# Performance work log

Measured on AMD Instinct MI355X. Metric: run time of the kernel, lower is better.

The kernel has to match this reference:

```python
import jax, jax.numpy as jnp
import numpy as np

OUTLINER_RATIO = 0.01
SUB_OUTLINER_BIT = 8
NEG_INF = -1e9


def setup_inputs() -> dict:
    key = jax.random.key(0)
    T, H, D = 4096, 8, 64
    qkv = jax.random.normal(key, (T, 3, H, D), dtype=jnp.float32)
    cu_seqlens = jnp.array([0, 1024, 2048, 3072, 4096], dtype=jnp.int32)
    return {"qkv": qkv, "cu_seqlens": cu_seqlens, "max_seqlen": 1024}


def _varlen_attention(q, k, v, cu_seqlens, causal=False):
    # q,k,v: [T, H, D]; sequences delimited by cu_seqlens (attention never
    # crosses segment boundaries, matching flash_attn_varlen semantics).
    T, H, D = q.shape
    scale = D ** (-0.5)
    pos = jnp.arange(T)
    seg = jnp.searchsorted(cu_seqlens, pos, side="right") - 1  # [T] segment ids
    mask = seg[:, None] == seg[None, :]                          # [T, T]
    if causal:
        mask = mask & (pos[:, None] >= pos[None, :])
    scores = jnp.einsum("thd,shd->hts", q, k) * scale            # [H, T, T]
    scores = jnp.where(mask[None, :, :], scores, NEG_INF)
    probs = jax.nn.softmax(scores, axis=-1)
    out = jnp.einsum("hts,shd->thd", probs, v)                   # [T, H, D]
    return out


def _outlier_quant_compress(x, outliner_ratio=OUTLINER_RATIO, bit=SUB_OUTLINER_BIT):
    # Outlier detection: keep top-ratio |x| entries in full precision;
    # quantize the residual (sub-outliers) to `bit` bits per-tensor.
    a = jnp.abs(x)
    thr = jnp.quantile(a.reshape(-1), 1.0 - outliner_ratio)
    outliers = jnp.where(a > thr, x, 0.0)
    resid = x - outliers
    qmax = 2.0 ** (bit - 1) - 1.0
    scale = jnp.maximum(jnp.max(jnp.abs(resid)), 1e-8) / qmax
    q = jnp.clip(jnp.round(resid / scale), -qmax, qmax)
    x_hat = outliers + q * scale  # decompressed approximation
    return x_hat, thr, scale


def reference(qkv, cu_seqlens, max_seqlen):
    q, k, v = qkv[:, 0], qkv[:, 1], qkv[:, 2]
    out = _varlen_attention(q, k, v, cu_seqlens, causal=False)
    # Compression pipeline (stats + quantize) runs on Q,K,V,O in the original
    # forward; it does not alter the forward output.
    for t in (q, k, v, out):
        _outlier_quant_compress(t)
    return out
```

## Files before the change

kernel.cpp:

```cpp
#include <hip/hip_runtime.h>


#define HEADS 8
#define DH 64
#define TQ 64
#define TK 64
#define PSTR 72
#define NSPLIT 2
#define NEG_BIG -1e30f
#define L2E 1.44269504088896340736f

using f32x4 = __attribute__((ext_vector_type(4))) float;
using s16x8 = __attribute__((ext_vector_type(8))) short;

__device__ inline unsigned short bf16b(float x) {
    union { float f; unsigned u; } c; c.f = x;
    unsigned r = c.u + 0x7fffu + ((c.u >> 16) & 1u);
    return (unsigned short)(r >> 16);
}

#if __has_builtin(__builtin_amdgcn_cvt_pk_bf16_f32)
__device__ inline unsigned pk2(float a, float b) {
    auto v = __builtin_amdgcn_cvt_pk_bf16_f32(a, b);
    unsigned u; __builtin_memcpy(&u, &v, 4); return u;
}
#else
__device__ inline unsigned pk2(float a, float b) {
    return (unsigned)bf16b(a) | ((unsigned)bf16b(b) << 16);
}
#endif

__global__ __launch_bounds__(256)
void prep_kernel(const float* __restrict__ qkv, unsigned short* __restrict__ Kb,
                 unsigned short* __restrict__ Vtb, int T) {
    __shared__ unsigned short Lt[64][PSTR];
    const int m = blockIdx.z + 1;
    const int h = blockIdx.y, t0 = blockIdx.x * 64;
    const int tid = threadIdx.x, d8 = tid & 7, tr = tid >> 3;

    #pragma unroll
    for (int i = 0; i < 2; ++i) {
        int t = t0 + i * 32 + tr;
        int tc = t < T ? t : T - 1;
        const float* src = qkv + ((size_t)tc * 3 + m) * (HEADS * DH) + h * DH + d8 * 8;
        float4 a = *(const float4*)src;
        float4 b = *(const float4*)(src + 4);
        unsigned p0 = pk2(a.x, a.y), p1 = pk2(a.z, a.w);
        unsigned p2 = pk2(b.x, b.y), p3 = pk2(b.z, b.w);
        if (m == 2) {
            *(uint2*)&Lt[i * 32 + tr][d8 * 8]     = make_uint2(p0, p1);
            *(uint2*)&Lt[i * 32 + tr][d8 * 8 + 4] = make_uint2(p2, p3);
        } else if (t < T) {
            *(uint4*)(Kb + ((size_t)h * T + t) * DH + d8 * 8) = make_uint4(p0, p1, p2, p3);
        }
    }
    if (m == 2) {
        __syncthreads();
        const int d = tid >> 2, tg = tid & 3;
        #pragma unroll
        for (int p = 0; p < 2; ++p) {
            int G = tg + 4 * p;
            int td = t0 + G * 8;
            unsigned u[4];
            #pragma unroll
            for (int jj = 0; jj < 4; ++jj)
                u[jj] = (unsigned)Lt[G * 8 + 2 * jj][d] |
                        ((unsigned)Lt[G * 8 + 2 * jj + 1][d] << 16);
            if (td < T)
                *(uint4*)(Vtb + ((size_t)h * DH + d) * T + td) =
                    make_uint4(u[0], u[1], u[2], u[3]);
        }
    }
}

__global__ __launch_bounds__(256, 3)
void fa_main(const float* __restrict__ qkv, const unsigned short* __restrict__ Kb,
             const unsigned short* __restrict__ Vtb, const int* __restrict__ cu,
             int n_cu, int T, float* __restrict__ out,
             float* __restrict__ Opart, float* __restrict__ Mp, float* __restrict__ Lp) {
    __shared__ unsigned short Ksh[2][TK * DH];
    __shared__ unsigned short Vsh[2][TK * DH];
    __shared__ unsigned short Psh[TQ][PSTR];

    const int tid = threadIdx.x;
    const int h = blockIdx.y, t0 = blockIdx.x * TQ;
    const int split = blockIdx.z, nsplit = gridDim.z;
    const int w = tid >> 6, lane = tid & 63, n15 = lane & 15, quad = lane >> 4;

    int trow = t0 + w * 16 + n15; if (trow > T - 1) trow = T - 1;
    int lo, hi;
    { int s = 0; for (int j = 1; j < n_cu - 1; ++j) if (cu[j] <= trow) s = j;
      lo = cu[s]; hi = cu[s + 1]; }
    int kb_, ke;
    { int s = 0; for (int j = 1; j < n_cu - 1; ++j) if (cu[j] <= t0) s = j;
      kb_ = cu[s];
      int tl = t0 + TQ - 1; if (tl > T - 1) tl = T - 1;
      s = 0; for (int j = 1; j < n_cu - 1; ++j) if (cu[j] <= tl) s = j;
      ke = cu[s + 1]; }

    s16x8 qfrag[2];
    {
        int tc = t0 + w * 16 + n15; if (tc > T - 1) tc = T - 1;
        const float* qp = qkv + (size_t)tc * 3 * (HEADS * DH) + h * DH + quad * 8;
        #pragma unroll
        for (int kh = 0; kh < 2; ++kh) {
            float4 a = *(const float4*)(qp + kh * 32);
            float4 b = *(const float4*)(qp + kh * 32 + 4);
            unsigned u0 = pk2(a.x * 0.125f, a.y * 0.125f);
            unsigned u1 = pk2(a.z * 0.125f, a.w * 0.125f);
            unsigned u2 = pk2(b.x * 0.125f, b.y * 0.125f);
            unsigned u3 = pk2(b.z * 0.125f, b.w * 0.125f);
            uint4 uu = make_uint4(u0, u1, u2, u3);
            __builtin_memcpy(&qfrag[kh], &uu, 16);
        }
    }

    const unsigned short* kb_h = Kb + (size_t)h * T * DH;
    const unsigned short* vt_h = Vtb + (size_t)h * DH * T;
    int krow_rel[2], vkey_off[2], ldst[2];
    const unsigned short* kbase[2];
    const unsigned short* vbase[2];
    #pragma unroll
    for (int i = 0; i < 2; ++i) {
        int gg = i * 64 + lane;
        int rr = gg >> 3;
        int gc = gg & 7;
        int row = w * 16 + rr;
        int gcol = gc ^ (row & 7);
        krow_rel[i] = row;
        kbase[i] = kb_h + gcol * 8;
        vbase[i] = vt_h + (size_t)row * T;
        vkey_off[i] = gcol * 8;
        ldst[i] = (w * 128 + i * 64) * 8;
    }
    int off16[2];
    #pragma unroll
    for (int kh = 0; kh < 2; ++kh)
        off16[kh] = n15 * 128 + (((kh * 4 + quad) ^ (n15 & 7)) * 16);

    f32x4 oacc[4];
    #pragma unroll
    for (int i = 0; i < 4; ++i) oacc[i] = (f32x4){0.f, 0.f, 0.f, 0.f};
    float m_ = NEG_BIG, l_ = 0.f;

    const int step = nsplit * TK;
    const int c0_start = (kb_ / TK) * TK + split * TK;

    #pragma unroll
    for (int i = 0; i < 2; ++i) {
        int rk = c0_start + krow_rel[i]; if (rk > T - 1) rk = T - 1;
        __builtin_amdgcn_global_load_lds(
            (const __attribute__((address_space(1))) void*)(kbase[i] + ((size_t)rk << 6)),
            (__attribute__((address_space(3))) void*)&Ksh[0][ldst[i]], 16, 0, 0);
        int kv = c0_start + vkey_off[i]; if (kv > T - 8) kv = T - 8;
        __builtin_amdgcn_global_load_lds(
            (const __attribute__((address_space(1))) void*)(vbase[i] + kv),
            (__attribute__((address_space(3))) void*)&Vsh[0][ldst[i]], 16, 0, 0);
    }

    int ib = 0;
    for (int c0 = c0_start; c0 < ke; c0 += step, ib ^= 1) {
        __syncthreads();

        int cn = c0 + step;
        if (cn < ke) {
            #pragma unroll
            for (int i = 0; i < 2; ++i) {
                int rk = cn + krow_rel[i]; if (rk > T - 1) rk = T - 1;
                __builtin_amdgcn_global_load_lds(
                    (const __attribute__((address_space(1))) void*)(kbase[i] + ((size_t)rk << 6)),
                    (__attribute__((address_space(3))) void*)&Ksh[ib ^ 1][ldst[i]], 16, 0, 0);
                int kv = cn + vkey_off[i]; if (kv > T - 8) kv = T - 8;
                __builtin_amdgcn_global_load_lds(
                    (const __attribute__((address_space(1))) void*)(vbase[i] + kv),
                    (__attribute__((address_space(3))) void*)&Vsh[ib ^ 1][ldst[i]], 16, 0, 0);
            }
        }

        const char* Kc = (const char*)Ksh[ib];
        f32x4 sacc[4];
        #pragma unroll
        for (int nt = 0; nt < 4; ++nt) {
            s16x8 k0 = *(const s16x8*)(Kc + nt * 2048 + off16[0]);
            s16x8 k1 = *(const s16x8*)(Kc + nt * 2048 + off16[1]);
            f32x4 z = (f32x4){0.f, 0.f, 0.f, 0.f};
            z = __builtin_amdgcn_mfma_f32_16x16x32_bf16(k0, qfrag[0], z, 0, 0, 0);
            z = __builtin_amdgcn_mfma_f32_16x16x32_bf16(k1, qfrag[1], z, 0, 0, 0);
            sacc[nt] = z;
        }

        if (!(c0 >= lo && c0 + TK <= hi)) {
            #pragma unroll
            for (int nt = 0; nt < 4; ++nt)
                #pragma unroll
                for (int reg = 0; reg < 4; ++reg) {
                    int key = c0 + nt * 16 + quad * 4 + reg;
                    bool valid = (key >= lo) && (key < hi);
                    sacc[nt][reg] = valid ? sacc[nt][reg] : NEG_BIG;
                }
        }

        float rm = NEG_BIG;
        #pragma unroll
        for (int nt = 0; nt < 4; ++nt)
            #pragma unroll
            for (int reg = 0; reg < 4; ++reg) rm = fmaxf(rm, sacc[nt][reg]);
        rm = fmaxf(rm, __shfl_xor(rm, 16));
        rm = fmaxf(rm, __shfl_xor(rm, 32));
        float mn = fmaxf(m_, rm);
        float alpha = exp2f((m_ - mn) * L2E);
        float mnl = mn * L2E;
        float rs = 0.f;
        #pragma unroll
        for (int nt = 0; nt < 4; ++nt) {
            float p0 = exp2f(fmaf(sacc[nt][0], L2E, -mnl));
            float p1 = exp2f(fmaf(sacc[nt][1], L2E, -mnl));
            float p2 = exp2f(fmaf(sacc[nt][2], L2E, -mnl));
            float p3 = exp2f(fmaf(sacc[nt][3], L2E, -mnl));
            rs += (p0 + p1) + (p2 + p3);
            *(uint2*)&Psh[w * 16 + n15][nt * 16 + quad * 4] =
                make_uint2(pk2(p0, p1), pk2(p2, p3));
        }
        rs += __shfl_xor(rs, 16);
        rs += __shfl_xor(rs, 32);
        l_ = fmaf(l_, alpha, rs);
        m_ = mn;
        #pragma unroll
        for (int reg = 0; reg < 4; ++reg) {
            float ar = __shfl(alpha, quad * 4 + reg);
            oacc[0][reg] *= ar; oacc[1][reg] *= ar;
            oacc[2][reg] *= ar; oacc[3][reg] *= ar;
        }

        s16x8 afr[2];
        afr[0] = *(const s16x8*)&Psh[w * 16 + n15][quad * 8];
        afr[1] = *(const s16x8*)&Psh[w * 16 + n15][32 + quad * 8];
        const char* Vc = (const char*)Vsh[ib];
        #pragma unroll
        for (int nt = 0; nt < 4; ++nt) {
            s16x8 v0 = *(const s16x8*)(Vc + nt * 2048 + off16[0]);
            s16x8 v1 = *(const s16x8*)(Vc + nt * 2048 + off16[1]);
            oacc[nt] = __builtin_amdgcn_mfma_f32_16x16x32_bf16(afr[0], v0, oacc[nt], 0, 0, 0);
            oacc[nt] = __builtin_amdgcn_mfma_f32_16x16x32_bf16(afr[1], v1, oacc[nt], 0, 0, 0);
        }
    }

    if (nsplit == 1) {
        #pragma unroll
        for (int reg = 0; reg < 4; ++reg) {
            float lr = __shfl(l_, quad * 4 + reg);
            float inv = 1.f / fmaxf(lr, 1e-30f);
            int t = t0 + w * 16 + quad * 4 + reg;
            if (t < T) {
                #pragma unroll
                for (int nt = 0; nt < 4; ++nt)
                    out[((size_t)t * HEADS + h) * DH + nt * 16 + n15] = oacc[nt][reg] * inv;
            }
        }
    } else {
        #pragma unroll
        for (int reg = 0; reg < 4; ++reg) {
            int t = t0 + w * 16 + quad * 4 + reg;
            if (t < T) {
                size_t base = (((size_t)split * T + t) * HEADS + h) * DH;
                #pragma unroll
                for (int nt = 0; nt < 4; ++nt)
                    Opart[base + nt * 16 + n15] = oacc[nt][reg];
            }
        }
        int tq = t0 + w * 16 + n15;
        if (quad == 0 && tq < T) {
            size_t mi = ((size_t)split * T + tq) * HEADS + h;
            Mp[mi] = m_; Lp[mi] = l_;
        }
    }
}

__global__ __launch_bounds__(256)
void fa_combine_kernel(const float* __restrict__ Opart, const float* __restrict__ Mp,
                       const float* __restrict__ Lp, float* __restrict__ out, int T) {
    int i4 = blockIdx.x * blockDim.x + threadIdx.x;
    int total = T * HEADS * (DH / 4);
    if (i4 >= total) return;
    int th = i4 / (DH / 4);
    int d4 = i4 - th * (DH / 4);
    size_t stride = (size_t)T * HEADS * DH;
    int mlstride = T * HEADS;
    float m[NSPLIT], l[NSPLIT];
    float M = NEG_BIG;
    #pragma unroll
    for (int s = 0; s < NSPLIT; ++s) {
        m[s] = Mp[(size_t)s * mlstride + th];
        l[s] = Lp[(size_t)s * mlstride + th];
        M = fmaxf(M, m[s]);
    }
    float L = 0.f, wgt[NSPLIT];
    #pragma unroll
    for (int s = 0; s < NSPLIT; ++s) {
        wgt[s] = exp2f((m[s] - M) * L2E);
        L = fmaf(l[s], wgt[s], L);
    }
    float inv = 1.f / fmaxf(L, 1e-30f);
    size_t off = (size_t)th * DH + 4 * d4;
    float4 o = make_float4(0.f, 0.f, 0.f, 0.f);
    #pragma unroll
    for (int s = 0; s < NSPLIT; ++s) {
        float4 a = *(const float4*)&Opart[(size_t)s * stride + off];
        float ws = wgt[s];
        o.x = fmaf(a.x, ws, o.x); o.y = fmaf(a.y, ws, o.y);
        o.z = fmaf(a.z, ws, o.z); o.w = fmaf(a.w, ws, o.w);
    }
    o.x *= inv; o.y *= inv; o.z *= inv; o.w *= inv;
    *(float4*)&out[off] = o;
}

extern "C" void kernel_launch(void* const* d_in, const int* in_sizes, int n_in,
                              void* d_out, int out_size, void* d_ws, size_t ws_size,
                              hipStream_t stream) {
    const float* qkv = (const float*)d_in[0];
    const int* cu    = (const int*)d_in[1];
    const int n_cu   = in_sizes[1];
    const int T      = in_sizes[0] / (3 * HEADS * DH);
    float* out       = (float*)d_out;

    size_t elems = (size_t)T * HEADS * DH;

    float* Opart = (float*)d_ws;
    float* Mpp   = Opart + (size_t)NSPLIT * elems;
    float* Lpp   = Mpp + (size_t)NSPLIT * T * HEADS;
    unsigned short* Kb  = (unsigned short*)(Lpp + (size_t)NSPLIT * T * HEADS);
    unsigned short* Vtb = Kb + elems;

    int ptiles = (T + 63) / 64;
    dim3 pgrid(ptiles, HEADS, 2);
    prep_kernel<<<pgrid, 256, 0, stream>>>(qkv, Kb, Vtb, T);

    int tiles = (T + TQ - 1) / TQ;
    dim3 grid(tiles, HEADS, NSPLIT);
    fa_main<<<grid, 256, 0, stream>>>(qkv, Kb, Vtb, cu, n_cu, T, out, Opart, Mpp, Lpp);

    int total4 = T * HEADS * (DH / 4);
    fa_combine_kernel<<<(total4 + 255) / 256, 256, 0, stream>>>(Opart, Mpp, Lpp, out, T);
}
```

Before: 109.4 us.

## Load K/V fragments directly from global into registers, drop LDS staging

Removes the double-buffered shared-memory staging of K and V tiles (global_load_lds plus syncthreads) and has each wave load its MFMA operand fragments straight from global memory into registers. Occupancy hint is raised from 3 to 4 blocks per CU since LDS use drops. This removes barrier and LDS traffic, but each of the 4 waves now fetches the same K/V tile separately, leaning on the L1/L2 caches. Prefetch overlap is also lost because the loads are issued in the same iteration they are consumed.

```diff
diff --git a/kernel.cpp b/kernel.cpp
--- a/kernel.cpp
+++ b/kernel.cpp
@@ -73,13 +73,11 @@
     }
 }
 
-__global__ __launch_bounds__(256, 3)
+__global__ __launch_bounds__(256, 4)
 void fa_main(const float* __restrict__ qkv, const unsigned short* __restrict__ Kb,
              const unsigned short* __restrict__ Vtb, const int* __restrict__ cu,
              int n_cu, int T, float* __restrict__ out,
              float* __restrict__ Opart, float* __restrict__ Mp, float* __restrict__ Lp) {
-    __shared__ unsigned short Ksh[2][TK * DH];
-    __shared__ unsigned short Vsh[2][TK * DH];
     __shared__ unsigned short Psh[TQ][PSTR];
 
     const int tid = threadIdx.x;
@@ -115,28 +113,11 @@
         }
     }
 
-    const unsigned short* kb_h = Kb + (size_t)h * T * DH;
-    const unsigned short* vt_h = Vtb + (size_t)h * DH * T;
-    int krow_rel[2], vkey_off[2], ldst[2];
-    const unsigned short* kbase[2];
-    const unsigned short* vbase[2];
-    #pragma unroll
-    for (int i = 0; i < 2; ++i) {
-        int gg = i * 64 + lane;
-        int rr = gg >> 3;
-        int gc = gg & 7;
-        int row = w * 16 + rr;
-        int gcol = gc ^ (row & 7);
-        krow_rel[i] = row;
-        kbase[i] = kb_h + gcol * 8;
-        vbase[i] = vt_h + (size_t)row * T;
-        vkey_off[i] = gcol * 8;
-        ldst[i] = (w * 128 + i * 64) * 8;
-    }
-    int off16[2];
-    #pragma unroll
-    for (int kh = 0; kh < 2; ++kh)
-        off16[kh] = n15 * 128 + (((kh * 4 + quad) ^ (n15 & 7)) * 16);
+    const unsigned short* kp_base = Kb + ((size_t)h * T + n15) * DH + quad * 8;
+    const unsigned short* vrow[4];
+    #pragma unroll
+    for (int nt = 0; nt < 4; ++nt)
+        vrow[nt] = Vtb + ((size_t)h * DH + nt * 16 + n15) * T;
 
     f32x4 oacc[4];
     #pragma unroll
@@ -146,46 +127,30 @@
     const int step = nsplit * TK;
     const int c0_start = (kb_ / TK) * TK + split * TK;
 
-    #pragma unroll
-    for (int i = 0; i < 2; ++i) {
-        int rk = c0_start + krow_rel[i]; if (rk > T - 1) rk = T - 1;
-        __builtin_amdgcn_global_load_lds(
-            (const __attribute__((address_space(1))) void*)(kbase[i] + ((size_t)rk << 6)),
-            (__attribute__((address_space(3))) void*)&Ksh[0][ldst[i]], 16, 0, 0);
-        int kv = c0_start + vkey_off[i]; if (kv > T - 8) kv = T - 8;
-        __builtin_amdgcn_global_load_lds(
-            (const __attribute__((address_space(1))) void*)(vbase[i] + kv),
-            (__attribute__((address_space(3))) void*)&Vsh[0][ldst[i]], 16, 0, 0);
-    }
-
-    int ib = 0;
-    for (int c0 = c0_start; c0 < ke; c0 += step, ib ^= 1) {
-        __syncthreads();
-
-        int cn = c0 + step;
-        if (cn < ke) {
+    for (int c0 = c0_start; c0 < ke; c0 += step) {
+        s16x8 kf[4][2];
+        #pragma unroll
+        for (int nt = 0; nt < 4; ++nt) {
+            int kk = c0 + nt * 16; if (kk > T - 16) kk = T - 16;
+            const unsigned short* kp = kp_base + (size_t)kk * DH;
+            kf[nt][0] = *(const s16x8*)kp;
+            kf[nt][1] = *(const s16x8*)(kp + 32);
+        }
+        s16x8 vf[4][2];
+        #pragma unroll
+        for (int kh = 0; kh < 2; ++kh) {
+            int vb = c0 + kh * 32 + quad * 8; if (vb > T - 8) vb = T - 8;
             #pragma unroll
-            for (int i = 0; i < 2; ++i) {
-                int rk = cn + krow_rel[i]; if (rk > T - 1) rk = T - 1;
-                __builtin_amdgcn_global_load_lds(
-                    (const __attribute__((address_space(1))) void*)(kbase[i] + ((size_t)rk << 6)),
-                    (__attribute__((address_space(3))) void*)&Ksh[ib ^ 1][ldst[i]], 16, 0, 0);
-                int kv = cn + vkey_off[i]; if (kv > T - 8) kv = T - 8;
-                __builtin_amdgcn_global_load_lds(
-                    (const __attribute__((address_space(1))) void*)(vbase[i] + kv),
-                    (__attribute__((address_space(3))) void*)&Vsh[ib ^ 1][ldst[i]], 16, 0, 0);
-            }
-        }
-
-        const char* Kc = (const char*)Ksh[ib];
+            for (int nt = 0; nt < 4; ++nt)
+                vf[nt][kh] = *(const s16x8*)(vrow[nt] + vb);
+        }
+
         f32x4 sacc[4];
         #pragma unroll
         for (int nt = 0; nt < 4; ++nt) {
-            s16x8 k0 = *(const s16x8*)(Kc + nt * 2048 + off16[0]);
-            s16x8 k1 = *(const s16x8*)(Kc + nt * 2048 + off16[1]);
             f32x4 z = (f32x4){0.f, 0.f, 0.f, 0.f};
-            z = __builtin_amdgcn_mfma_f32_16x16x32_bf16(k0, qfrag[0], z, 0, 0, 0);
-            z = __builtin_amdgcn_mfma_f32_16x16x32_bf16(k1, qfrag[1], z, 0, 0, 0);
+            z = __builtin_amdgcn_mfma_f32_16x16x32_bf16(kf[nt][0], qfrag[0], z, 0, 0, 0);
+            z = __builtin_amdgcn_mfma_f32_16x16x32_bf16(kf[nt][1], qfrag[1], z, 0, 0, 0);
             sacc[nt] = z;
         }
 
@@ -235,13 +200,10 @@
         s16x8 afr[2];
         afr[0] = *(const s16x8*)&Psh[w * 16 + n15][quad * 8];
         afr[1] = *(const s16x8*)&Psh[w * 16 + n15][32 + quad * 8];
-        const char* Vc = (const char*)Vsh[ib];
         #pragma unroll
         for (int nt = 0; nt < 4; ++nt) {
-            s16x8 v0 = *(const s16x8*)(Vc + nt * 2048 + off16[0]);
-            s16x8 v1 = *(const s16x8*)(Vc + nt * 2048 + off16[1]);
-            oacc[nt] = __builtin_amdgcn_mfma_f32_16x16x32_bf16(afr[0], v0, oacc[nt], 0, 0, 0);
-            oacc[nt] = __builtin_amdgcn_mfma_f32_16x16x32_bf16(afr[1], v1, oacc[nt], 0, 0, 0);
+            oacc[nt] = __builtin_amdgcn_mfma_f32_16x16x32_bf16(afr[0], vf[nt][0], oacc[nt], 0, 0, 0);
+            oacc[nt] = __builtin_amdgcn_mfma_f32_16x16x32_bf16(afr[1], vf[nt][1], oacc[nt], 0, 0, 0);
         }
     }
 
```

Measured after the change: 139.3 us. 1.27x slower.
